# Kernel optimization log

Hardware: AMD Instinct MI355X
Metric: run time of the kernel (lower is better)

The kernel has to match this reference:

```python
import jax, jax.numpy as jnp
import numpy as np
from jax import lax

B, H_ENC, E, H, V, T = 64, 512, 512, 1024, 32000, 64
SOS, EOS = 1, 2


def setup_inputs() -> dict:
    key = jax.random.key(0)
    ks = jax.random.split(key, 7)
    s = 0.05
    return {
        "encoder_hidden": jax.random.normal(ks[0], (2, B, H_ENC), jnp.float32),
        "embedding": jax.random.normal(ks[1], (V, E), jnp.float32) * s,
        "Wh_w": jax.random.normal(ks[2], (H, 2 * H_ENC), jnp.float32) * s,
        "Wh_b": jnp.zeros((H,), jnp.float32),
        "W_ih": jax.random.normal(ks[3], (3 * H, E + 2 * H_ENC), jnp.float32) * s,
        "W_hh": jax.random.normal(ks[4], (3 * H, H), jnp.float32) * s,
        "b_ih": jnp.zeros((3 * H,), jnp.float32),
        "b_hh": jnp.zeros((3 * H,), jnp.float32),
        "out_w": jax.random.normal(ks[5], (V, H), jnp.float32) * s,
        "out_b": jnp.zeros((V,), jnp.float32),
    }


def reference(encoder_hidden, embedding, Wh_w, Wh_b, W_ih, W_hh, b_ih, b_hh, out_w, out_b):
    # initialize_forward: [2,B,H_enc] -> transpose -> [B,2,H_enc] -> reshape [1,B,2*H_enc] -> Wh
    flat = encoder_hidden.transpose(1, 0, 2).reshape(B, 2 * H_ENC)  # [B, 1024]
    h0 = flat @ Wh_w.T + Wh_b  # [B, H]
    # _get_context: hidden[-2:] permuted -> [B,2,H_enc] -> reshape [B, 2*H_enc] (constant per step)
    context = flat  # same flattening, num_layers of encoder hidden == 2 (bidirectional)

    def gru_cell(x, h):
        # PyTorch GRU cell: gates order (r, z, n)
        gi = x @ W_ih.T + b_ih  # [B, 3H]
        gh = h @ W_hh.T + b_hh  # [B, 3H]
        i_r, i_z, i_n = jnp.split(gi, 3, axis=-1)
        h_r, h_z, h_n = jnp.split(gh, 3, axis=-1)
        r = jax.nn.sigmoid(i_r + h_r)
        z = jax.nn.sigmoid(i_z + h_z)
        n = jnp.tanh(i_n + r * h_n)
        return (1.0 - z) * n + z * h

    def step(carry, _):
        inp, h, finished = carry  # inp [B] int32, h [B,H], finished [B] bool
        x = embedding[inp]  # [B, E]
        gru_in = jnp.concatenate([x, context], axis=-1)  # [B, E + 2*H_enc]
        h = gru_cell(gru_in, h)
        logits = h @ out_w.T + out_b  # [B, V]  (dropout p=0 -> identity)
        tok = jnp.argmax(logits, axis=-1).astype(jnp.int32)  # topk k=1 greedy
        finished = finished | (tok == EOS)
        inp_next = jnp.where(finished, EOS, tok)  # masked_fill with eos
        return (inp_next, h, finished), tok

    init = (jnp.full((B,), SOS, jnp.int32), h0, jnp.zeros((B,), bool))
    (inp, h_final, fin), toks = lax.scan(step, init, None, length=T)  # toks [T, B]
    decoder_outputs = toks.T  # [B, T]  (torch.stack(outputs).T)
    decoder_hidden = h_final[None]  # [1, B, H]
    return decoder_outputs, decoder_hidden
```

## Files before the change

### kernel.cpp

```cpp
#include <hip/hip_runtime.h>
#include <math.h>

#define BB   64
#define HENC 512
#define EE   512
#define HH   1024
#define VV   32000
#define TT   64
#define G3   3072
#define SOS_TOK 1
#define EOS_TOK 2
#define KSEG 128
#define NP2  4000
#define GHB  192
#define LOGB 500

typedef __attribute__((ext_vector_type(8))) short short8;
typedef __attribute__((ext_vector_type(8))) unsigned short ushort8;
typedef __attribute__((ext_vector_type(4))) float f32x4;
typedef unsigned short ushort;
typedef unsigned int uint;

#define OFF_FLATT 0u
#define OFF_XT    65536u
#define OFF_HT    98304u
#define OFF_GC    163840u
#define OFF_P     360448u
#define OFF_PH    1933312u
#define OFF_PMAX  2457600u
#define OFF_PIDX  2713600u
#define OFF_FIN   2969600u
#define OFF_HA    2969728u
#define OFF_HB    3002496u
#define OFF_WB    3068032u
#define OFF_END   19452032u
#define NEED_BYTES ((size_t)OFF_END * 4u)

#define NEG_INF (-3.402823466e38f)
#define IDX_INF 0x7fffffff

__device__ __forceinline__ ushort f2bf(float x) {
  uint u = __float_as_uint(x);
  u = u + 0x7fffu + ((u >> 16) & 1u);
  return (ushort)(u >> 16);
}

#define BETTER(av, ai, bv, bi) ((av) > (bv) || ((av) == (bv) && (ai) < (bi)))

__global__ __launch_bounds__(256) void k_setup(const float* __restrict__ enc,
                                               const float* __restrict__ emb,
                                               float* __restrict__ flatT,
                                               float* __restrict__ xT,
                                               int* __restrict__ fin0) {
  int idx = blockIdx.x * 256 + threadIdx.x;
  int j = idx >> 6, b = idx & 63;
  float v = (j < 512) ? enc[b * 512 + j] : enc[32768 + b * 512 + (j - 512)];
  flatT[j * 64 + b] = v;
  if (j < 512) xT[j * 64 + b] = emb[SOS_TOK * EE + j];
  if (idx < 64) fin0[idx] = 0;
}

__global__ __launch_bounds__(256) void k_packWb(const float* __restrict__ W,
                                                ushort* __restrict__ Wb) {
  int t = blockIdx.x * 256 + threadIdx.x;
  int l = t & 63, kc = (t >> 6) & 31, nt = t >> 11;
  int n = nt * 16 + (l & 15);
  int k = kc * 32 + ((l >> 4) << 3);
  const float* src = W + (size_t)n * 1024 + k;
  ushort8 r;
  #pragma unroll
  for (int j = 0; j < 8; ++j) r[j] = f2bf(src[j]);
  *(ushort8*)(Wb + (size_t)t * 8) = r;
}

__global__ __launch_bounds__(256) void k_gemm(const float* __restrict__ AT,
                                              const float* __restrict__ W,
                                              int ldw, int wofs,
                                              float* __restrict__ C, int N) {
  __shared__ float Ws[KSEG][65];
  int tid = threadIdx.x;
  int n0 = blockIdx.x * 64;
  int k0 = blockIdx.y * KSEG;

  #pragma unroll
  for (int r = 0; r < 8; ++r) {
    int f4 = tid + 256 * r;
    int n = f4 >> 5, kq = f4 & 31;
    float4 w4 = *(const float4*)&W[(size_t)(n0 + n) * ldw + wofs + k0 + 4 * kq];
    Ws[4 * kq + 0][n] = w4.x;
    Ws[4 * kq + 1][n] = w4.y;
    Ws[4 * kq + 2][n] = w4.z;
    Ws[4 * kq + 3][n] = w4.w;
  }
  __syncthreads();

  int wv = __builtin_amdgcn_readfirstlane(tid >> 6);
  int lane = tid & 63;
  int mb = wv * 16;

  float acc[16];
  #pragma unroll
  for (int i = 0; i < 16; ++i) acc[i] = 0.f;

  #pragma unroll 4
  for (int kk = 0; kk < KSEG; ++kk) {
    float w = Ws[kk][lane];
    const float* a = &AT[(size_t)(k0 + kk) * 64 + mb];
    float av[16];
    *(float4*)&av[0]  = *(const float4*)(a + 0);
    *(float4*)&av[4]  = *(const float4*)(a + 4);
    *(float4*)&av[8]  = *(const float4*)(a + 8);
    *(float4*)&av[12] = *(const float4*)(a + 12);
    #pragma unroll
    for (int i = 0; i < 16; ++i) acc[i] += av[i] * w;
  }

  float* dst = C + ((size_t)blockIdx.y * 64 + mb) * N + n0 + lane;
  #pragma unroll
  for (int i = 0; i < 16; ++i) dst[(size_t)i * N] = acc[i];
}

__global__ __launch_bounds__(256) void k_gates(const float* __restrict__ xT,
                                               const float* __restrict__ hT,
                                               const float* __restrict__ Wih,
                                               const float* __restrict__ Whh,
                                               float* __restrict__ P,
                                               int base_by) {
  __shared__ float Ws[KSEG][65];
  int tid = threadIdx.x;
  int n0 = blockIdx.x * 64;
  int by = blockIdx.y + base_by;
  bool gi = (by < 4);
  const float* AT = gi ? xT : hT;
  const float* W  = gi ? Wih : Whh;
  int ldw = gi ? 1536 : 1024;
  int nsegs = gi ? 1 : 2;
  int k0base = gi ? by * KSEG : (by - 4) * 256;

  int wv = __builtin_amdgcn_readfirstlane(tid >> 6);
  int lane = tid & 63;
  int mb = wv * 16;

  float acc[16];
  #pragma unroll
  for (int i = 0; i < 16; ++i) acc[i] = 0.f;

  for (int s = 0; s < nsegs; ++s) {
    int k0 = k0base + s * KSEG;
    if (s) __syncthreads();
    #pragma unroll
    for (int r = 0; r < 8; ++r) {
      int f4 = tid + 256 * r;
      int n = f4 >> 5, kq = f4 & 31;
      float4 w4 = *(const float4*)&W[(size_t)(n0 + n) * ldw + k0 + 4 * kq];
      Ws[4 * kq + 0][n] = w4.x;
      Ws[4 * kq + 1][n] = w4.y;
      Ws[4 * kq + 2][n] = w4.z;
      Ws[4 * kq + 3][n] = w4.w;
    }
    __syncthreads();
    #pragma unroll 4
    for (int kk = 0; kk < KSEG; ++kk) {
      float w = Ws[kk][lane];
      const float* a = &AT[(size_t)(k0 + kk) * 64 + mb];
      float av[16];
      *(float4*)&av[0]  = *(const float4*)(a + 0);
      *(float4*)&av[4]  = *(const float4*)(a + 4);
      *(float4*)&av[8]  = *(const float4*)(a + 8);
      *(float4*)&av[12] = *(const float4*)(a + 12);
      #pragma unroll
      for (int i = 0; i < 16; ++i) acc[i] += av[i] * w;
    }
  }

  float* dst = P + ((size_t)by * 64 + mb) * G3 + n0 + lane;
  #pragma unroll
  for (int i = 0; i < 16; ++i) dst[(size_t)i * G3] = acc[i];
}

__global__ __launch_bounds__(256) void k_reduce_gc(const float* __restrict__ P,
                                                   const float* __restrict__ b_ih,
                                                   float* __restrict__ gc) {
  int idx = blockIdx.x * 256 + threadIdx.x;
  int n = idx % G3;
  float s = b_ih[n];
  #pragma unroll
  for (int p = 0; p < 8; ++p) s += P[(size_t)p * (64 * G3) + idx];
  gc[idx] = s;
}

__device__ __forceinline__ void packH1(float v, int b, int g, ushort* hA) {
  int kc = g >> 5, q = (g >> 3) & 3, j = g & 7;
  int lane = (q << 4) | (b & 15), mt = b >> 4;
  size_t fi = ((size_t)((mt * 32 + kc) * 64 + lane)) * 8 + j;
  hA[fi] = f2bf(v);
}

__global__ __launch_bounds__(256) void k_reduce_h0(const float* __restrict__ Ph,
                                                   const float* __restrict__ Wh_b,
                                                   float* __restrict__ hT,
                                                   float* __restrict__ hB,
                                                   ushort* __restrict__ hA) {
  int idx = blockIdx.x * 256 + threadIdx.x;
  int b = idx >> 10, g = idx & 1023;
  float s = Wh_b[g];
  #pragma unroll
  for (int p = 0; p < 8; ++p) s += Ph[(size_t)p * 65536 + idx];
  hT[g * 64 + b] = s;
  hB[idx] = s;
  packH1(s, b, g, hA);
}

__global__ __launch_bounds__(256) void k_combine(const float* __restrict__ P,
                                                 const float* __restrict__ gc,
                                                 const float* __restrict__ b_hh,
                                                 float* __restrict__ hT,
                                                 float* __restrict__ hB,
                                                 ushort* __restrict__ hA) {
  int b = blockIdx.x >> 2;
  int g = ((blockIdx.x & 3) << 8) + threadIdx.x;
  float ir = gc[b * G3 + g];
  float iz = gc[b * G3 + 1024 + g];
  float in_ = gc[b * G3 + 2048 + g];
  float hr = b_hh[g], hz = b_hh[1024 + g], hn = b_hh[2048 + g];
  #pragma unroll
  for (int p = 0; p < 4; ++p) {
    const float* row = P + ((size_t)p * 64 + b) * G3;
    ir += row[g]; iz += row[1024 + g]; in_ += row[2048 + g];
  }
  #pragma unroll
  for (int p = 4; p < 8; ++p) {
    const float* row = P + ((size_t)p * 64 + b) * G3;
    hr += row[g]; hz += row[1024 + g]; hn += row[2048 + g];
  }
  float rr = 1.f / (1.f + expf(-(ir + hr)));
  float zz = 1.f / (1.f + expf(-(iz + hz)));
  float nn = tanhf(in_ + rr * hn);
  float hold = hT[g * 64 + b];
  float hnew = (1.f - zz) * nn + zz * hold;
  hT[g * 64 + b] = hnew;
  hB[b * 1024 + g] = hnew;
  packH1(hnew, b, g, hA);
}

__device__ __forceinline__ short8 cvt8(const float* p) {
  float4 x = *(const float4*)p;
  float4 y = *(const float4*)(p + 4);
  short8 r;
  r[0] = (short)f2bf(x.x); r[1] = (short)f2bf(x.y);
  r[2] = (short)f2bf(x.z); r[3] = (short)f2bf(x.w);
  r[4] = (short)f2bf(y.x); r[5] = (short)f2bf(y.y);
  r[6] = (short)f2bf(y.z); r[7] = (short)f2bf(y.w);
  return r;
}

template <bool PACKED>
__global__ __launch_bounds__(256) void k_logits(const ushort* __restrict__ Wb,
                                                const float* __restrict__ Wf,
                                                const ushort* __restrict__ hA,
                                                const float* __restrict__ bo,
                                                float* __restrict__ pmax,
                                                int* __restrict__ pidx,
                                                const float* __restrict__ hT,
                                                const float* __restrict__ Whh,
                                                float* __restrict__ P) {
  __shared__ float Ws[KSEG][65];
  int tid = threadIdx.x, wv = tid >> 6, lane = tid & 63;

  if (blockIdx.x < GHB) {
    int bx = blockIdx.x;
    int by = bx / 48;
    int n0 = (bx % 48) * 64;
    int slot = 4 + by;
    int k0base = by * 256;

    int wvs = __builtin_amdgcn_readfirstlane(wv);
    int mb = wvs * 16;

    float acc[16];
    #pragma unroll
    for (int i = 0; i < 16; ++i) acc[i] = 0.f;

    for (int s = 0; s < 2; ++s) {
      int k0 = k0base + s * KSEG;
      if (s) __syncthreads();
      #pragma unroll
      for (int r = 0; r < 8; ++r) {
        int f4 = tid + 256 * r;
        int n = f4 >> 5, kq = f4 & 31;
        float4 w4 = *(const float4*)&Whh[(size_t)(n0 + n) * 1024 + k0 + 4 * kq];
        Ws[4 * kq + 0][n] = w4.x;
        Ws[4 * kq + 1][n] = w4.y;
        Ws[4 * kq + 2][n] = w4.z;
        Ws[4 * kq + 3][n] = w4.w;
      }
      __syncthreads();
      #pragma unroll 4
      for (int kk = 0; kk < KSEG; ++kk) {
        float w = Ws[kk][lane];
        const float* a = &hT[(size_t)(k0 + kk) * 64 + mb];
        float av[16];
        *(float4*)&av[0]  = *(const float4*)(a + 0);
        *(float4*)&av[4]  = *(const float4*)(a + 4);
        *(float4*)&av[8]  = *(const float4*)(a + 8);
        *(float4*)&av[12] = *(const float4*)(a + 12);
        #pragma unroll
        for (int i = 0; i < 16; ++i) acc[i] += av[i] * w;
      }
    }

    float* dst = P + ((size_t)slot * 64 + mb) * G3 + n0 + lane;
    #pragma unroll
    for (int i = 0; i < 16; ++i) dst[(size_t)i * G3] = acc[i];
    return;
  }

  int nt = (blockIdx.x - GHB) * 4 + wv;
  int nl = lane & 15, q = lane >> 4;

  const short8* Bp = (const short8*)Wb + ((size_t)nt * 2048 + lane);
  const float*  Bf = Wf + (size_t)(nt * 16 + nl) * 1024 + (q << 3);
  const short8* Ap = (const short8*)hA + lane;

  f32x4 acc[4];
  #pragma unroll
  for (int m = 0; m < 4; ++m) acc[m] = (f32x4){0.f, 0.f, 0.f, 0.f};

  short8 bR[4], aR[4][4];
  #pragma unroll
  for (int d = 0; d < 4; ++d) {
    bR[d] = PACKED ? Bp[d * 64] : cvt8(Bf + d * 32);
    #pragma unroll
    for (int m = 0; m < 4; ++m) aR[d][m] = Ap[(m * 32 + d) * 64];
  }

  #pragma unroll
  for (int kc = 0; kc < 32; ++kc) {
    const int sl = kc & 3;
    #pragma unroll
    for (int m = 0; m < 4; ++m)
      acc[m] = __builtin_amdgcn_mfma_f32_16x16x32_bf16(aR[sl][m], bR[sl], acc[m], 0, 0, 0);
    if (kc < 28) {
      bR[sl] = PACKED ? Bp[(kc + 4) * 64] : cvt8(Bf + (kc + 4) * 32);
      #pragma unroll
      for (int m = 0; m < 4; ++m) aR[sl][m] = Ap[(m * 32 + kc + 4) * 64];
    }
  }

  float bias = bo[nt * 16 + nl];
  int myn = nt * 16 + nl;
  #pragma unroll
  for (int mt = 0; mt < 4; ++mt) {
    #pragma unroll
    for (int r = 0; r < 4; ++r) {
      float v1 = acc[mt][r] + bias; int i1 = myn;
      float v2 = NEG_INF;           int i2 = IDX_INF;
      #pragma unroll
      for (int s = 1; s < 16; s <<= 1) {
        float ov1 = __shfl_xor(v1, s, 64); int oi1 = __shfl_xor(i1, s, 64);
        float ov2 = __shfl_xor(v2, s, 64); int oi2 = __shfl_xor(i2, s, 64);
        bool take = BETTER(ov1, oi1, v1, i1);
        float n1v = take ? ov1 : v1; int n1i = take ? oi1 : i1;
        float cav = take ? v1 : ov1; int cai = take ? i1 : oi1;
        float cbv = take ? ov2 : v2; int cbi = take ? oi2 : i2;
        bool bb = BETTER(cbv, cbi, cav, cai);
        v1 = n1v; i1 = n1i;
        v2 = bb ? cbv : cav; i2 = bb ? cbi : cai;
      }
      if (nl == 0) {
        int m = mt * 16 + q * 4 + r;
        pmax[(size_t)m * NP2 + nt * 2 + 0] = v1;
        pidx[(size_t)m * NP2 + nt * 2 + 0] = i1;
        pmax[(size_t)m * NP2 + nt * 2 + 1] = v2;
        pidx[(size_t)m * NP2 + nt * 2 + 1] = i2;
      }
    }
  }
}

__global__ __launch_bounds__(256) void k_finish(const float* __restrict__ pmax,
                                                const int* __restrict__ pidx,
                                                const float* __restrict__ hB,
                                                const float* __restrict__ Wf,
                                                const float* __restrict__ bo,
                                                const float* __restrict__ emb,
                                                const int* __restrict__ fin_old,
                                                int* __restrict__ fin_new,
                                                float* __restrict__ xT,
                                                float* __restrict__ tok_out, int t) {
  __shared__ float  sv[16];
  __shared__ int    si[16];
  __shared__ int    sch[4];
  __shared__ double ssc[4];
  __shared__ int    sinp;
  int b = blockIdx.x, tid = threadIdx.x;
  int wv = tid >> 6, ln = tid & 63;

  float v0 = NEG_INF, v1 = NEG_INF, v2 = NEG_INF, v3 = NEG_INF;
  int   i0 = IDX_INF, i1 = IDX_INF, i2 = IDX_INF, i3 = IDX_INF;

  #define INS4(cv, ci)                                                   \
    {                                                                    \
      bool c0 = BETTER(cv, ci, v0, i0);                                  \
      bool c1 = BETTER(cv, ci, v1, i1);                                  \
      bool c2 = BETTER(cv, ci, v2, i2);                                  \
      bool c3 = BETTER(cv, ci, v3, i3);                                  \
      v3 = c3 ? (c2 ? v2 : (cv)) : v3;  i3 = c3 ? (c2 ? i2 : (ci)) : i3; \
      v2 = c2 ? (c1 ? v1 : (cv)) : v2;  i2 = c2 ? (c1 ? i1 : (ci)) : i2; \
      v1 = c1 ? (c0 ? v0 : (cv)) : v1;  i1 = c1 ? (c0 ? i0 : (ci)) : i1; \
      v0 = c0 ? (cv) : v0;              i0 = c0 ? (ci) : i0;             \
    }

  if (tid < 250) {
    const float* pm = pmax + (size_t)b * NP2 + tid * 16;
    const int*   pi = pidx + (size_t)b * NP2 + tid * 16;
    #pragma unroll
    for (int j4 = 0; j4 < 4; ++j4) {
      float4 c4 = *(const float4*)(pm + j4 * 4);
      int4   x4 = *(const int4*)(pi + j4 * 4);
      INS4(c4.x, x4.x);
      INS4(c4.y, x4.y);
      INS4(c4.z, x4.z);
      INS4(c4.w, x4.w);
    }
  }

  #define CESW(xv, xi, yv, yi)                                     \
    {                                                              \
      bool sw_ = BETTER(yv, yi, xv, xi);                           \
      float tv_ = xv; int ti_ = xi;                                \
      xv = sw_ ? yv : xv;  xi = sw_ ? yi : xi;                     \
      yv = sw_ ? tv_ : yv; yi = sw_ ? ti_ : yi;                    \
    }

  for (int s = 1; s < 64; s <<= 1) {
    float w0 = __shfl_xor(v0, s, 64), w1 = __shfl_xor(v1, s, 64);
    float w2 = __shfl_xor(v2, s, 64), w3 = __shfl_xor(v3, s, 64);
    int   j0 = __shfl_xor(i0, s, 64), j1 = __shfl_xor(i1, s, 64);
    int   j2 = __shfl_xor(i2, s, 64), j3 = __shfl_xor(i3, s, 64);
    if (BETTER(w3, j3, v0, i0)) { v0 = w3; i0 = j3; }
    if (BETTER(w2, j2, v1, i1)) { v1 = w2; i1 = j2; }
    if (BETTER(w1, j1, v2, i2)) { v2 = w1; i2 = j1; }
    if (BETTER(w0, j0, v3, i3)) { v3 = w0; i3 = j0; }
    CESW(v0, i0, v2, i2);
    CESW(v1, i1, v3, i3);
    CESW(v0, i0, v1, i1);
    CESW(v2, i2, v3, i3);
  }

  if (ln == 0) {
    sv[wv * 4 + 0] = v0; si[wv * 4 + 0] = i0;
    sv[wv * 4 + 1] = v1; si[wv * 4 + 1] = i1;
    sv[wv * 4 + 2] = v2; si[wv * 4 + 2] = i2;
    sv[wv * 4 + 3] = v3; si[wv * 4 + 3] = i3;
  }
  __syncthreads();

  if (tid == 0) {
    float t0 = NEG_INF, t1 = NEG_INF, t2 = NEG_INF, t3 = NEG_INF;
    int   x0 = IDX_INF, x1 = IDX_INF, x2 = IDX_INF, x3 = IDX_INF;
    #pragma unroll
    for (int e = 0; e < 16; ++e) {
      float cv = sv[e]; int ci = si[e];
      bool c0 = BETTER(cv, ci, t0, x0);
      bool c1 = BETTER(cv, ci, t1, x1);
      bool c2 = BETTER(cv, ci, t2, x2);
      bool c3 = BETTER(cv, ci, t3, x3);
      t3 = c3 ? (c2 ? t2 : cv) : t3;  x3 = c3 ? (c2 ? x2 : ci) : x3;
      t2 = c2 ? (c1 ? t1 : cv) : t2;  x2 = c2 ? (c1 ? x1 : ci) : x2;
      t1 = c1 ? (c0 ? t0 : cv) : t1;  x1 = c1 ? (c0 ? x0 : ci) : x1;
      t0 = c0 ? cv : t0;              x0 = c0 ? ci : x0;
    }
    sch[0] = x0; sch[1] = x1; sch[2] = x2; sch[3] = x3;
  }
  __syncthreads();

  int c = wv;
  int cid = sch[c];
  const float4* hv4 = (const float4*)(hB + (size_t)b * 1024);
  const float4* wv4 = (const float4*)(Wf + (size_t)cid * 1024);
  double s = 0.0;
  #pragma unroll
  for (int j = 0; j < 4; ++j) {
    float4 hx = hv4[j * 64 + ln];
    float4 wx = wv4[j * 64 + ln];
    s += (double)hx.x * (double)wx.x + (double)hx.y * (double)wx.y +
         (double)hx.z * (double)wx.z + (double)hx.w * (double)wx.w;
  }
  #pragma unroll
  for (int sh = 1; sh < 64; sh <<= 1) s += __shfl_xor(s, sh, 64);
  if (ln == 0) ssc[c] = s + (double)bo[cid];
  __syncthreads();

  if (tid == 0) {
    double bs = ssc[0]; int bid = sch[0];
    #pragma unroll
    for (int j = 1; j < 4; ++j)
      if (ssc[j] > bs || (ssc[j] == bs && sch[j] < bid)) { bs = ssc[j]; bid = sch[j]; }
    int tok = bid;
    int f = fin_old[b] | (tok == EOS_TOK ? 1 : 0);
    tok_out[b * TT + t] = (float)tok;
    fin_new[b] = f;
    sinp = f ? EOS_TOK : tok;
  }
  __syncthreads();
  int inp = sinp;
  xT[tid * 64 + b]         = emb[(size_t)inp * EE + tid];
  xT[(tid + 256) * 64 + b] = emb[(size_t)inp * EE + tid + 256];
}

__global__ __launch_bounds__(256) void k_hout(const float* __restrict__ hB,
                                              float* __restrict__ outH) {
  int idx = blockIdx.x * 256 + threadIdx.x;
  outH[idx] = hB[idx];
}

extern "C" void kernel_launch(void* const* d_in, const int* in_sizes, int n_in,
                              void* d_out, int out_size, void* d_ws, size_t ws_size,
                              hipStream_t stream) {
  const float* enc   = (const float*)d_in[0];
  const float* emb   = (const float*)d_in[1];
  const float* Wh_w  = (const float*)d_in[2];
  const float* Wh_b  = (const float*)d_in[3];
  const float* W_ih  = (const float*)d_in[4];
  const float* W_hh  = (const float*)d_in[5];
  const float* b_ih  = (const float*)d_in[6];
  const float* b_hh  = (const float*)d_in[7];
  const float* out_w = (const float*)d_in[8];
  const float* out_b = (const float*)d_in[9];

  float* ws    = (float*)d_ws;
  float* flatT = ws + OFF_FLATT;
  float* xT    = ws + OFF_XT;
  float* hT    = ws + OFF_HT;
  float* gc    = ws + OFF_GC;
  float* P     = ws + OFF_P;
  float* Ph    = ws + OFF_PH;
  float* pmax  = ws + OFF_PMAX;
  int*   pidx  = (int*)(ws + OFF_PIDX);
  int*   fin   = (int*)(ws + OFF_FIN);
  ushort* hA   = (ushort*)(ws + OFF_HA);
  float* hB    = ws + OFF_HB;
  ushort* Wb   = (ushort*)(ws + OFF_WB);

  float* outTok = (float*)d_out;
  float* outH   = (float*)d_out + BB * TT;

  const bool packed = (ws_size >= NEED_BYTES);

  k_setup<<<256, 256, 0, stream>>>(enc, emb, flatT, xT, fin);
  if (packed) k_packWb<<<16000, 256, 0, stream>>>(out_w, Wb);
  k_gemm<<<dim3(48, 8), 256, 0, stream>>>(flatT, W_ih, 1536, 512, P, G3);
  k_reduce_gc<<<768, 256, 0, stream>>>(P, b_ih, gc);
  k_gemm<<<dim3(16, 8), 256, 0, stream>>>(flatT, Wh_w, 1024, 0, Ph, HH);
  k_reduce_h0<<<256, 256, 0, stream>>>(Ph, Wh_b, hT, hB, hA);
  k_gates<<<dim3(48, 4), 256, 0, stream>>>(xT, hT, W_ih, W_hh, P, 4);

  for (int t = 0; t < TT; ++t) {
    k_gates<<<dim3(48, 4), 256, 0, stream>>>(xT, hT, W_ih, W_hh, P, 0);
    k_combine<<<256, 256, 0, stream>>>(P, gc, b_hh, hT, hB, hA);
    if (packed)
      k_logits<true><<<LOGB + GHB, 256, 0, stream>>>(Wb, out_w, hA, out_b, pmax, pidx,
                                                     hT, W_hh, P);
    else
      k_logits<false><<<LOGB + GHB, 256, 0, stream>>>(Wb, out_w, hA, out_b, pmax, pidx,
                                                      hT, W_hh, P);
    k_finish<<<64, 256, 0, stream>>>(pmax, pidx, hB, out_w, out_b, emb,
                                     fin + (t & 1) * 64, fin + ((t + 1) & 1) * 64,
                                     xT, outTok, t);
  }
  k_hout<<<256, 256, 0, stream>>>(hB, outH);
}
```

Baseline: 3.934 ms.

## Fuse GRU gate combine into k_gates via last-block atomic counter

Removes the separate k_combine launch from each decode step. Each k_gates block bumps a per-column-group atomic counter, and the last of the 12 contributing blocks reduces the partial gate sums. That block then applies the GRU nonlinearity and writes hT, hB and the packed bf16 hA, using float4-vectorised loads. This trades one kernel launch and its dependency gap per step for a serialized tail, where only 16 blocks do the combine work, plus atomic and threadfence overhead.

Measured after the change: 4.656 ms. +18.4%, slower.

```diff
diff --git a/kernel.cpp b/kernel.cpp
--- a/kernel.cpp
+++ b/kernel.cpp
@@ -33,7 +33,8 @@
 #define OFF_HA    2969728u
 #define OFF_HB    3002496u
 #define OFF_WB    3068032u
-#define OFF_END   19452032u
+#define OFF_CNT   19452032u
+#define OFF_END   19452048u
 #define NEED_BYTES ((size_t)OFF_END * 4u)
 
 #define NEG_INF (-3.402823466e38f)
@@ -51,13 +52,15 @@
                                                const float* __restrict__ emb,
                                                float* __restrict__ flatT,
                                                float* __restrict__ xT,
-                                               int* __restrict__ fin0) {
+                                               int* __restrict__ fin0,
+                                               int* __restrict__ cnt) {
   int idx = blockIdx.x * 256 + threadIdx.x;
   int j = idx >> 6, b = idx & 63;
   float v = (j < 512) ? enc[b * 512 + j] : enc[32768 + b * 512 + (j - 512)];
   flatT[j * 64 + b] = v;
   if (j < 512) xT[j * 64 + b] = emb[SOS_TOK * EE + j];
   if (idx < 64) fin0[idx] = 0;
+  if (idx < 16) cnt[idx] = 0;
 }
 
 __global__ __launch_bounds__(256) void k_packWb(const float* __restrict__ W,
@@ -125,8 +128,14 @@
                                                const float* __restrict__ Wih,
                                                const float* __restrict__ Whh,
                                                float* __restrict__ P,
-                                               int base_by) {
+                                               int base_by,
+                                               const float* __restrict__ gc,
+                                               const float* __restrict__ b_hh,
+                                               float* __restrict__ hB,
+                                               ushort* __restrict__ hA,
+                                               int* __restrict__ cnt) {
   __shared__ float Ws[KSEG][65];
+  __shared__ int sLast;
   int tid = threadIdx.x;
   int n0 = blockIdx.x * 64;
   int by = blockIdx.y + base_by;
@@ -176,6 +185,90 @@
   float* dst = P + ((size_t)by * 64 + mb) * G3 + n0 + lane;
   #pragma unroll
   for (int i = 0; i < 16; ++i) dst[(size_t)i * G3] = acc[i];
+
+  if (base_by != 0) return;
+
+  int j = blockIdx.x & 15;
+  __syncthreads();
+  if (tid == 0) {
+    __threadfence();
+    sLast = (atomicAdd(&cnt[j], 1) == 11) ? 1 : 0;
+  }
+  __syncthreads();
+  if (!sLast) return;
+  __threadfence();
+
+  int g0 = j * 64;
+  int g  = g0 + (tid & 15) * 4;
+  int bb = (tid >> 4) * 4;
+
+  #define ADD4(a, q) { a.x += (q).x; a.y += (q).y; a.z += (q).z; a.w += (q).w; }
+  #define GRUC(irc, izc, inc, hrc, hzc, hnc, holdc, out)            \
+    {                                                               \
+      float rr = 1.f / (1.f + expf(-((irc) + (hrc))));              \
+      float zz = 1.f / (1.f + expf(-((izc) + (hzc))));              \
+      float nn = tanhf((inc) + rr * (hnc));                         \
+      out = (1.f - zz) * nn + zz * (holdc);                         \
+    }
+
+  float4 hr0 = *(const float4*)&b_hh[g];
+  float4 hz0 = *(const float4*)&b_hh[1024 + g];
+  float4 hn0 = *(const float4*)&b_hh[2048 + g];
+
+  #pragma unroll
+  for (int ib = 0; ib < 4; ++ib) {
+    int b = bb + ib;
+    const float* gcb = gc + (size_t)b * G3;
+    float4 ir  = *(const float4*)&gcb[g];
+    float4 iz  = *(const float4*)&gcb[1024 + g];
+    float4 in_ = *(const float4*)&gcb[2048 + g];
+    float4 hr = hr0, hz = hz0, hn = hn0;
+    #pragma unroll
+    for (int p = 0; p < 4; ++p) {
+      const float* row = P + ((size_t)p * 64 + b) * G3;
+      float4 a0 = *(const float4*)&row[g];
+      float4 a1 = *(const float4*)&row[1024 + g];
+      float4 a2 = *(const float4*)&row[2048 + g];
+      ADD4(ir, a0); ADD4(iz, a1); ADD4(in_, a2);
+    }
+    #pragma unroll
+    for (int p = 4; p < 8; ++p) {
+      const float* row = P + ((size_t)p * 64 + b) * G3;
+      float4 a0 = *(const float4*)&row[g];
+      float4 a1 = *(const float4*)&row[1024 + g];
+      float4 a2 = *(const float4*)&row[2048 + g];
+      ADD4(hr, a0); ADD4(hz, a1); ADD4(hn, a2);
+    }
+    float4 hold = *(const float4*)&hB[(size_t)b * 1024 + g];
+    float4 h;
+    GRUC(ir.x, iz.x, in_.x, hr.x, hz.x, hn.x, hold.x, h.x);
+    GRUC(ir.y, iz.y, in_.y, hr.y, hz.y, hn.y, hold.y, h.y);
+    GRUC(ir.z, iz.z, in_.z, hr.z, hz.z, hn.z, hold.z, h.z);
+    GRUC(ir.w, iz.w, in_.w, hr.w, hz.w, hn.w, hold.w, h.w);
+
+    *(float4*)&hB[(size_t)b * 1024 + g] = h;
+    float* ht = (float*)&((float*)0)[0];
+    (void)ht;
+    ((float*)P != nullptr) ? (void)0 : (void)0;
+    {
+      float* hTw = const_cast<float*>(hT);
+      hTw[(size_t)(g + 0) * 64 + b] = h.x;
+      hTw[(size_t)(g + 1) * 64 + b] = h.y;
+      hTw[(size_t)(g + 2) * 64 + b] = h.z;
+      hTw[(size_t)(g + 3) * 64 + b] = h.w;
+    }
+    {
+      int kc = g >> 5, q = (g >> 3) & 3, j0 = g & 7;
+      int lane_a = (q << 4) | (b & 15), mt = b >> 4;
+      size_t fi = ((size_t)((mt * 32 + kc) * 64 + lane_a)) * 8 + j0;
+      ushort4 u;
+      u.x = f2bf(h.x); u.y = f2bf(h.y); u.z = f2bf(h.z); u.w = f2bf(h.w);
+      *(ushort4*)(hA + fi) = u;
+    }
+  }
+
+  __syncthreads();
+  if (tid == 0) atomicExch(&cnt[j], 0);
 }
 
 __global__ __launch_bounds__(256) void k_reduce_gc(const float* __restrict__ P,
@@ -209,38 +302,6 @@
   hT[g * 64 + b] = s;
   hB[idx] = s;
   packH1(s, b, g, hA);
-}
-
-__global__ __launch_bounds__(256) void k_combine(const float* __restrict__ P,
-                                                 const float* __restrict__ gc,
-                                                 const float* __restrict__ b_hh,
-                                                 float* __restrict__ hT,
-                                                 float* __restrict__ hB,
-                                                 ushort* __restrict__ hA) {
-  int b = blockIdx.x >> 2;
-  int g = ((blockIdx.x & 3) << 8) + threadIdx.x;
-  float ir = gc[b * G3 + g];
-  float iz = gc[b * G3 + 1024 + g];
-  float in_ = gc[b * G3 + 2048 + g];
-  float hr = b_hh[g], hz = b_hh[1024 + g], hn = b_hh[2048 + g];
-  #pragma unroll
-  for (int p = 0; p < 4; ++p) {
-    const float* row = P + ((size_t)p * 64 + b) * G3;
-    ir += row[g]; iz += row[1024 + g]; in_ += row[2048 + g];
-  }
-  #pragma unroll
-  for (int p = 4; p < 8; ++p) {
-    const float* row = P + ((size_t)p * 64 + b) * G3;
-    hr += row[g]; hz += row[1024 + g]; hn += row[2048 + g];
-  }
-  float rr = 1.f / (1.f + expf(-(ir + hr)));
-  float zz = 1.f / (1.f + expf(-(iz + hz)));
-  float nn = tanhf(in_ + rr * hn);
-  float hold = hT[g * 64 + b];
-  float hnew = (1.f - zz) * nn + zz * hold;
-  hT[g * 64 + b] = hnew;
-  hB[b * 1024 + g] = hnew;
-  packH1(hnew, b, g, hA);
 }
 
 __device__ __forceinline__ short8 cvt8(const float* p) {
@@ -547,18 +608,20 @@
   float* outH   = (float*)d_out + BB * TT;
 
   const bool packed = (ws_size >= NEED_BYTES);
-
-  k_setup<<<256, 256, 0, stream>>>(enc, emb, flatT, xT, fin);
+  int* cnt = (int*)(ws + (packed ? OFF_CNT : OFF_WB));
+
+  k_setup<<<256, 256, 0, stream>>>(enc, emb, flatT, xT, fin, cnt);
   if (packed) k_packWb<<<16000, 256, 0, stream>>>(out_w, Wb);
   k_gemm<<<dim3(48, 8), 256, 0, stream>>>(flatT, W_ih, 1536, 512, P, G3);
   k_reduce_gc<<<768, 256, 0, stream>>>(P, b_ih, gc);
   k_gemm<<<dim3(16, 8), 256, 0, stream>>>(flatT, Wh_w, 1024, 0, Ph, HH);
   k_reduce_h0<<<256, 256, 0, stream>>>(Ph, Wh_b, hT, hB, hA);
-  k_gates<<<dim3(48, 4), 256, 0, stream>>>(xT, hT, W_ih, W_hh, P, 4);
+  k_gates<<<dim3(48, 4), 256, 0, stream>>>(xT, hT, W_ih, W_hh, P, 4,
+                                           gc, b_hh, hB, hA, cnt);
 
   for (int t = 0; t < TT; ++t) {
-    k_gates<<<dim3(48, 4), 256, 0, stream>>>(xT, hT, W_ih, W_hh, P, 0);
-    k_combine<<<256, 256, 0, stream>>>(P, gc, b_hh, hT, hB, hA);
+    k_gates<<<dim3(48, 4), 256, 0, stream>>>(xT, hT, W_ih, W_hh, P, 0,
+                                             gc, b_hh, hB, hA, cnt);
     if (packed)
       k_logits<true><<<LOGB + GHB, 256, 0, stream>>>(Wb, out_w, hA, out_b, pmax, pidx,
                                                      hT, W_hh, P);
```
